# Optimization experiments

Measured on AMD Instinct MI355X. Metric: run time of the kernel, lower is better.

## Reference

```python
import jax, jax.numpy as jnp
import numpy as np

N = 8192   # nodes per graph batch
D = 128    # node_feat_dim
E = 131072 # edges per graph batch
B = 64     # graphs per batch


def _linear_init(k, fin, fout):
    s = 1.0 / np.sqrt(fin)
    kw, kb = jax.random.split(k)
    W = jax.random.uniform(kw, (fin, fout), jnp.float32, -s, s)
    b = jax.random.uniform(kb, (fout,), jnp.float32, -s, s)
    return W, b


def setup_inputs() -> dict:
    key = jax.random.key(0)
    ks = jax.random.split(key, 10)
    x1 = jax.random.normal(ks[0], (N, D), jnp.float32)
    x2 = jax.random.normal(ks[1], (N, D), jnp.float32)
    edge_index1 = jax.random.randint(ks[2], (2, E), 0, N)
    edge_index2 = jax.random.randint(ks[3], (2, E), 0, N)
    # block-contiguous graph ids; every graph id present on both sides
    batch = jnp.arange(N, dtype=jnp.int32) // (N // B)
    mW1, mb1 = _linear_init(ks[4], 2 * D, 512)
    mW2, mb2 = _linear_init(ks[5], 512, 256)  # 256 == 2*D (update_net constraint)
    uW1, ub1 = _linear_init(ks[6], 4 * D, 512)
    uW2, ub2 = _linear_init(ks[7], 512, 256)
    uW3, ub3 = _linear_init(ks[8], 256, D)
    return dict(x1=x1, edge_index1=edge_index1, batch1=batch,
                x2=x2, edge_index2=edge_index2, batch2=batch,
                mW1=mW1, mb1=mb1, mW2=mW2, mb2=mb2,
                uW1=uW1, ub1=ub1, uW2=uW2, ub2=ub2, uW3=uW3, ub3=ub3)


def _message_aggr(x, edge_index, mW1, mb1, mW2, mb2):
    tgt, src = edge_index[0], edge_index[1]
    inp = jnp.concatenate([x[src], x[tgt]], axis=-1)          # [E, 2D]
    msg = jax.nn.relu(inp @ mW1 + mb1) @ mW2 + mb2            # [E, 2D]
    return jax.ops.segment_sum(msg, tgt, num_segments=x.shape[0])


def _cross_attention(x1, batch1, x2, batch2):
    scores = x1 @ x2.T                                        # [N1, N2]
    mask = batch1[:, None] == batch2[None, :]
    scores = jnp.where(mask, scores, -jnp.inf)
    att1 = x1 - jax.nn.softmax(scores, axis=1) @ x2
    att2 = x2 - jax.nn.softmax(scores, axis=0).T @ x1
    return att1, att2


def _node_update(x, messages, attentions, uW1, ub1, uW2, ub2, uW3, ub3):
    u = jnp.concatenate([messages, attentions, x], axis=-1)   # [N, 4D]
    h = jax.nn.relu(u @ uW1 + ub1)
    h = jax.nn.relu(h @ uW2 + ub2)
    return x + h @ uW3 + ub3                                  # residual update


def reference(x1, edge_index1, batch1, x2, edge_index2, batch2,
              mW1, mb1, mW2, mb2, uW1, ub1, uW2, ub2, uW3, ub3):
    m1 = _message_aggr(x1, edge_index1, mW1, mb1, mW2, mb2)
    m2 = _message_aggr(x2, edge_index2, mW1, mb1, mW2, mb2)
    a1, a2 = _cross_attention(x1, batch1, x2, batch2)
    new_x1 = _node_update(x1, m1, a1, uW1, ub1, uW2, ub2, uW3, ub3)
    new_x2 = _node_update(x2, m2, a2, uW1, ub1, uW2, ub2, uW3, ub3)
    return new_x1, new_x2
```

## Files before the change

### kernel.cpp

```cpp
#include <hip/hip_runtime.h>
#include <stdint.h>


typedef unsigned short u16;
typedef __bf16 bf16x8 __attribute__((ext_vector_type(8)));
typedef float f32x4 __attribute__((ext_vector_type(4)));

#define NN 8192
#define DD 128
#define EE 131072
#define GS 128
#define NG 64

__device__ __forceinline__ float bf2f(u16 u){
  return __uint_as_float(((uint32_t)u) << 16);
}
__device__ __forceinline__ u16 f2bf(float f){
  uint32_t x = __float_as_uint(f);
  return (u16)((x + 0x7fffu + ((x >> 16) & 1u)) >> 16);
}
__device__ __forceinline__ void gload16(const u16* g, u16* l){
  __builtin_amdgcn_global_load_lds(
      (const __attribute__((address_space(1))) uint32_t*)(uintptr_t)g,
      (__attribute__((address_space(3))) uint32_t*)(uintptr_t)l, 16, 0, 0);
}
template<int N>
__device__ __forceinline__ void wbar(){
  if constexpr (N == 0)      asm volatile("s_waitcnt vmcnt(0)" ::: "memory");
  else if constexpr (N == 1) asm volatile("s_waitcnt vmcnt(1)" ::: "memory");
  else if constexpr (N == 2) asm volatile("s_waitcnt vmcnt(2)" ::: "memory");
  else if constexpr (N == 4) asm volatile("s_waitcnt vmcnt(4)" ::: "memory");
  __builtin_amdgcn_s_barrier();
  __builtin_amdgcn_sched_barrier(0);
}
__device__ __forceinline__ void bar(){
  __builtin_amdgcn_s_barrier();
  __builtin_amdgcn_sched_barrier(0);
}

__device__ __forceinline__ void pq_gemm(
    const u16* __restrict__ A, const u16* __restrict__ Wt,
    const float* __restrict__ bias, u16* __restrict__ out,
    int bx, int by, u16* __restrict__ sh, int t)
{
  u16* As = sh;
  u16* Bs = sh + 16384;
  const int brow = by << 7, bcol = bx << 7;
  const int w = t >> 6, lane = t & 63;
  const int rb = (w >> 1) << 6, cb = (w & 1) << 6;
  const int lr = lane & 15, lq = lane >> 4;

  #pragma unroll
  for (int i = 0; i < 8; i++){
    int sg = i * 256 + t;
    int r = sg >> 4, p = sg & 15;
    int l = p ^ (r & 7);
    gload16(A  + (size_t)(brow + r) * 128 + (l << 3), As + sg * 8);
    gload16(Wt + (size_t)(bcol + r) * 128 + (l << 3), Bs + sg * 8);
  }
  wbar<0>();

  f32x4 acc[4][4];
  #pragma unroll
  for (int i = 0; i < 4; i++)
    #pragma unroll
    for (int j = 0; j < 4; j++) acc[i][j] = (f32x4){0.f, 0.f, 0.f, 0.f};

  #pragma unroll
  for (int kb = 0; kb < 4; kb++){
    bf16x8 af[4], bfr[4];
    #pragma unroll
    for (int mi = 0; mi < 4; mi++){
      int row = rb + mi * 16 + lr;
      af[mi] = *(const bf16x8*)&As[(row << 7) + ((((kb << 2) | lq) ^ (row & 7)) << 3)];
    }
    #pragma unroll
    for (int ni = 0; ni < 4; ni++){
      int row = cb + ni * 16 + lr;
      bfr[ni] = *(const bf16x8*)&Bs[(row << 7) + ((((kb << 2) | lq) ^ (row & 7)) << 3)];
    }
    #pragma unroll
    for (int mi = 0; mi < 4; mi++)
      #pragma unroll
      for (int ni = 0; ni < 4; ni++)
        acc[mi][ni] = __builtin_amdgcn_mfma_f32_16x16x32_bf16(af[mi], bfr[ni], acc[mi][ni], 0, 0, 0);
  }

  #pragma unroll
  for (int mi = 0; mi < 4; mi++)
    #pragma unroll
    for (int ni = 0; ni < 4; ni++)
      #pragma unroll
      for (int rr = 0; rr < 4; rr++){
        int grow = brow + rb + mi * 16 + lq * 4 + rr;
        int gcol = bcol + cb + ni * 16 + lr;
        out[(size_t)grow * 1024 + gcol] = f2bf(acc[mi][ni][rr] + bias[gcol]);
      }
}

__global__ __launch_bounds__(256)
void pre_k(const float* __restrict__ mW1, const float* __restrict__ mb1,
           const float* __restrict__ mW2, const float* __restrict__ uW1,
           const float* __restrict__ uW2, const float* __restrict__ uW3,
           const float* __restrict__ x1, const float* __restrict__ x2,
           const int* __restrict__ ei1, const int* __restrict__ ei2,
           u16* __restrict__ WtPQ, float* __restrict__ bPQ,
           u16* __restrict__ Wtm2, u16* __restrict__ Wtu1,
           u16* __restrict__ Wtu2, u16* __restrict__ Wtu3,
           u16* __restrict__ xb, u16* __restrict__ xt,
           u16* __restrict__ U, int* __restrict__ deg)
{
  __shared__ u16 T[8704];
  int b = blockIdx.x, t = threadIdx.x;
  if (b < 168){
    const float* srcs[6] = {mW1, mW1 + 128 * 512, mW2, uW1, uW2, uW3};
    u16* dsts[6] = {WtPQ, WtPQ + 512 * 128, Wtm2, Wtu1, Wtu2, Wtu3};
    const int ldSs[6] = {512, 512, 256, 512, 256, 128};
    const int ldDs[6] = {128, 128, 512, 512, 512, 256};
    const int jb[7]   = {0, 16, 32, 64, 128, 160, 168};
    int j = 0;
    while (b >= jb[j + 1]) j++;
    const int l = b - jb[j];
    const int ldS = ldSs[j], ldD = ldDs[j];
    const int ntc = ldS >> 6;
    const int k0 = (l / ntc) << 6, c0 = (l % ntc) << 6;
    const float* S = srcs[j];
    u16* D = dsts[j];
    #pragma unroll
    for (int i = 0; i < 4; i++){
      int s = i * 256 + t;
      int r = s >> 4, c4 = (s & 15) << 2;
      float4 v = *(const float4*)&S[(size_t)(k0 + r) * ldS + c0 + c4];
      uint2 pk;
      pk.x = (uint32_t)f2bf(v.x) | ((uint32_t)f2bf(v.y) << 16);
      pk.y = (uint32_t)f2bf(v.z) | ((uint32_t)f2bf(v.w) << 16);
      *(uint2*)&T[r * 68 + c4] = pk;
    }
    __syncthreads();
    #pragma unroll
    for (int i = 0; i < 4; i++){
      int s = i * 256 + t;
      int c = s >> 4, k4 = (s & 15) << 2;
      uint32_t a0 = T[(k4 + 0) * 68 + c];
      uint32_t a1 = T[(k4 + 1) * 68 + c];
      uint32_t a2 = T[(k4 + 2) * 68 + c];
      uint32_t a3 = T[(k4 + 3) * 68 + c];
      uint2 pk; pk.x = a0 | (a1 << 16); pk.y = a2 | (a3 << 16);
      *(uint2*)&D[(size_t)(c0 + c) * ldD + k0 + k4] = pk;
    }
  } else if (b == 168){
    #pragma unroll
    for (int i = 0; i < 4; i++){
      int idx = i * 256 + t;
      bPQ[idx] = (idx < 512) ? 0.f : mb1[idx - 512];
    }
  } else if (b < 2217){
    int a = b - 169;
    int side = a >> 10, blk = a & 1023;
    const float* x = side ? x2 : x1;
    int i4 = blk * 256 + t;
    float4 v = *(const float4*)&x[(size_t)i4 * 4];
    uint2 pk;
    pk.x = (uint32_t)f2bf(v.x) | ((uint32_t)f2bf(v.y) << 16);
    pk.y = (uint32_t)f2bf(v.z) | ((uint32_t)f2bf(v.w) << 16);
    *(uint2*)&xb[(size_t)side * NN * DD + (size_t)i4 * 4] = pk;
    int n = i4 >> 5, d = (i4 << 2) & 127;
    *(uint2*)&U[((size_t)side * NN + n) * 512 + 384 + d] = pk;
  } else if (b < 2473){
    int a = b - 2217;
    int side = a >> 7, blk = a & 127;
    const float* x = side ? x2 : x1;
    u16* dst = xt + (size_t)side * DD * NN;
    const int n0 = blk * 64;
    #pragma unroll
    for (int i = 0; i < 8; i++){
      int s = i * 256 + t;
      int r = s >> 5, c4 = (s & 31) << 2;
      float4 v = *(const float4*)&x[(size_t)(n0 + r) * DD + c4];
      uint2 pk;
      pk.x = (uint32_t)f2bf(v.x) | ((uint32_t)f2bf(v.y) << 16);
      pk.y = (uint32_t)f2bf(v.z) | ((uint32_t)f2bf(v.w) << 16);
      *(uint2*)&T[r * 136 + c4] = pk;
    }
    __syncthreads();
    #pragma unroll
    for (int i = 0; i < 8; i++){
      int s = i * 256 + t;
      int d = s >> 4, n4 = (s & 15) << 2;
      uint32_t a0 = T[(n4 + 0) * 136 + d];
      uint32_t a1 = T[(n4 + 1) * 136 + d];
      uint32_t a2 = T[(n4 + 2) * 136 + d];
      uint32_t a3 = T[(n4 + 3) * 136 + d];
      uint2 pk; pk.x = a0 | (a1 << 16); pk.y = a2 | (a3 << 16);
      *(uint2*)(dst + (size_t)d * NN + n0 + n4) = pk;
    }
  } else {
    int a = b - 2473;
    int side = a >> 9, blk = a & 511;
    const int* ei = side ? ei2 : ei1;
    int e = blk * 256 + t;
    atomicAdd(&deg[side * NN + ei[e]], 1);
  }
}

__global__ __launch_bounds__(256)
void scan_k(const int* __restrict__ deg,
            int* __restrict__ offs1, int* __restrict__ cur1,
            int* __restrict__ offs2, int* __restrict__ cur2){
  const int* d = deg + blockIdx.x * NN;
  int* offs = blockIdx.x ? offs2 : offs1;
  int* cur  = blockIdx.x ? cur2  : cur1;
  __shared__ int part[256];
  const int t = threadIdx.x;
  const int base = t * 32;
  int loc[32];
  int s = 0;
  #pragma unroll
  for (int i = 0; i < 32; i++){ loc[i] = s; s += d[base + i]; }
  part[t] = s;
  __syncthreads();
  for (int off = 1; off < 256; off <<= 1){
    int v = (t >= off) ? part[t - off] : 0;
    __syncthreads();
    part[t] += v;
    __syncthreads();
  }
  int pre = (t == 0) ? 0 : part[t - 1];
  #pragma unroll
  for (int i = 0; i < 32; i++){
    int o = pre + loc[i];
    offs[base + i] = o;
    cur[base + i]  = o;
  }
  if (t == 255) offs[NN] = part[255];
}

__global__ __launch_bounds__(256)
void mid_k(const u16* __restrict__ xb, const u16* __restrict__ WtPQ,
           const float* __restrict__ bPQ, u16* __restrict__ PQ,
           const int* __restrict__ ei1, const int* __restrict__ ei2,
           int* __restrict__ cur1, int* __restrict__ cur2,
           int* __restrict__ srt1, int* __restrict__ srt2,
           const u16* __restrict__ xt, u16* __restrict__ U)
{
  __shared__ u16 sh[32768];
  const int b = blockIdx.x, t = threadIdx.x;
  if (b < 1024){
    pq_gemm(xb, WtPQ, bPQ, PQ, b >> 7, b & 127, sh, t);
    return;
  }
  if (b < 2048){
    int a = b - 1024;
    int side = a >> 9, blk = a & 511;
    const int* ei = side ? ei2 : ei1;
    int* cur = side ? cur2 : cur1;
    int* srt = side ? srt2 : srt1;
    int e = blk * 256 + t;
    int tgt = ei[e], src = ei[EE + e];
    int p = atomicAdd(&cur[tgt], 1);
    srt[p] = src;
    return;
  }
  const int a = b - 2048;
  const int side = a >> 7;
  const int g = a & 63, h = (a >> 6) & 1;
  const u16* Xa = xb + (size_t)side * NN * DD;
  const u16* Xb = xb + (size_t)(1 - side) * NN * DD;
  const u16* Xt = xt + (size_t)(1 - side) * DD * NN;
  u16* Uside = U + (size_t)side * NN * 512;

  u16* XaS = sh;
  u16* XbS = sh + 8704;

  const int w = t >> 6, lane = t & 63;
  const int lr = lane & 15, lq = lane >> 4;

  {
    const u16* sa = Xa + ((size_t)g * GS + h * 64) * DD;
    #pragma unroll
    for (int i = 0; i < 4; i++){
      int s = i * 256 + t; int r = s >> 4, c8 = (s & 15) << 3;
      *(uint4*)&XaS[r * 136 + c8] = *(const uint4*)(sa + (size_t)r * DD + c8);
    }
    const u16* sb = Xb + (size_t)g * GS * DD;
    #pragma unroll
    for (int i = 0; i < 8; i++){
      int s = i * 256 + t; int r = s >> 4, c8 = (s & 15) << 3;
      *(uint4*)&XbS[r * 136 + c8] = *(const uint4*)(sb + (size_t)r * DD + c8);
    }
  }
  __syncthreads();

  f32x4 sc[8];
  #pragma unroll
  for (int ct = 0; ct < 8; ct++) sc[ct] = (f32x4){0.f, 0.f, 0.f, 0.f};
  #pragma unroll
  for (int kb = 0; kb < 4; kb++){
    bf16x8 aa = *(const bf16x8*)&XaS[(w * 16 + lr) * 136 + kb * 32 + (lq << 3)];
    #pragma unroll
    for (int ct = 0; ct < 8; ct++){
      bf16x8 bb = *(const bf16x8*)&XbS[(ct * 16 + lr) * 136 + kb * 32 + (lq << 3)];
      sc[ct] = __builtin_amdgcn_mfma_f32_16x16x32_bf16(aa, bb, sc[ct], 0, 0, 0);
    }
  }
  float inv[4];
  #pragma unroll
  for (int rr = 0; rr < 4; rr++){
    float m = sc[0][rr];
    #pragma unroll
    for (int ct = 1; ct < 8; ct++) m = fmaxf(m, sc[ct][rr]);
    #pragma unroll
    for (int sh_ = 1; sh_ < 16; sh_ <<= 1) m = fmaxf(m, __shfl_xor(m, sh_, 64));
    float s = 0.f;
    #pragma unroll
    for (int ct = 0; ct < 8; ct++){
      float e = __expf(sc[ct][rr] - m);
      sc[ct][rr] = e; s += e;
    }
    #pragma unroll
    for (int sh_ = 1; sh_ < 16; sh_ <<= 1) s += __shfl_xor(s, sh_, 64);
    inv[rr] = 1.f / s;
  }
  #pragma unroll
  for (int ct = 0; ct < 8; ct++)
    #pragma unroll
    for (int rr = 0; rr < 4; rr++)
      XaS[(w * 16 + lq * 4 + rr) * 136 + ct * 16 + lr] = f2bf(sc[ct][rr] * inv[rr]);
  __syncthreads();

  f32x4 o[8];
  #pragma unroll
  for (int ct = 0; ct < 8; ct++) o[ct] = (f32x4){0.f, 0.f, 0.f, 0.f};
  #pragma unroll
  for (int kb = 0; kb < 4; kb++){
    bf16x8 aa = *(const bf16x8*)&XaS[(w * 16 + lr) * 136 + kb * 32 + (lq << 3)];
    #pragma unroll
    for (int ct = 0; ct < 8; ct++){
      bf16x8 bb = *(const bf16x8*)(Xt + (size_t)(ct * 16 + lr) * NN + g * GS + kb * 32 + (lq << 3));
      o[ct] = __builtin_amdgcn_mfma_f32_16x16x32_bf16(aa, bb, o[ct], 0, 0, 0);
    }
  }
  const u16* XaG = Xa + ((size_t)g * GS + h * 64) * DD;
  #pragma unroll
  for (int ct = 0; ct < 8; ct++)
    #pragma unroll
    for (int rr = 0; rr < 4; rr++){
      int row = w * 16 + lq * 4 + rr, col = ct * 16 + lr;
      float xa = bf2f(XaG[(size_t)row * DD + col]);
      Uside[((size_t)g * GS + h * 64 + row) * 512 + 256 + col] = f2bf(xa - o[ct][rr]);
    }
}

__global__ __launch_bounds__(256)
void gather_k(const int* __restrict__ offs1, const int* __restrict__ srt1,
              const int* __restrict__ offs2, const int* __restrict__ srt2,
              const u16* __restrict__ PQ, u16* __restrict__ S)
{
  const int side = blockIdx.y;
  const int* offs = side ? offs2 : offs1;
  const int* srt  = side ? srt2  : srt1;
  const u16* base = PQ + (size_t)side * NN * 1024;
  u16* Sb = S + (size_t)side * NN * 512;

  const int node = (blockIdx.x << 2) + (threadIdx.x >> 6);
  const int lane = threadIdx.x & 63;
  const int beg = offs[node], end = offs[node + 1];
  const u16* lbase = base + (lane << 3);

  uint4 qv = *(const uint4*)(base + (size_t)node * 1024 + 512 + (lane << 3));
  float q[8];
  {
    uint32_t qw[4] = {qv.x, qv.y, qv.z, qv.w};
    #pragma unroll
    for (int i = 0; i < 4; i++){
      q[i * 2]     = bf2f((u16)(qw[i] & 0xffffu));
      q[i * 2 + 1] = bf2f((u16)(qw[i] >> 16));
    }
  }
  float acc[8] = {0.f,0.f,0.f,0.f,0.f,0.f,0.f,0.f};

  int e = beg;
  for (; e + 15 < end; e += 16){
    int sx[16];
    #pragma unroll
    for (int i = 0; i < 16; i++) sx[i] = srt[e + i];
    uint4 pv[16];
    #pragma unroll
    for (int i = 0; i < 16; i++)
      pv[i] = *(const uint4*)(lbase + (size_t)sx[i] * 1024);
    #pragma unroll
    for (int i = 0; i < 16; i++){
      uint32_t w0[4] = {pv[i].x, pv[i].y, pv[i].z, pv[i].w};
      #pragma unroll
      for (int j = 0; j < 4; j++){
        acc[j*2]   += fmaxf(bf2f((u16)(w0[j] & 0xffffu)) + q[j*2],   0.f);
        acc[j*2+1] += fmaxf(bf2f((u16)(w0[j] >> 16))     + q[j*2+1], 0.f);
      }
    }
  }
  for (; e + 7 < end; e += 8){
    int sx[8];
    #pragma unroll
    for (int i = 0; i < 8; i++) sx[i] = srt[e + i];
    uint4 pv[8];
    #pragma unroll
    for (int i = 0; i < 8; i++)
      pv[i] = *(const uint4*)(lbase + (size_t)sx[i] * 1024);
    #pragma unroll
    for (int i = 0; i < 8; i++){
      uint32_t w0[4] = {pv[i].x, pv[i].y, pv[i].z, pv[i].w};
      #pragma unroll
      for (int j = 0; j < 4; j++){
        acc[j*2]   += fmaxf(bf2f((u16)(w0[j] & 0xffffu)) + q[j*2],   0.f);
        acc[j*2+1] += fmaxf(bf2f((u16)(w0[j] >> 16))     + q[j*2+1], 0.f);
      }
    }
  }
  for (; e + 3 < end; e += 4){
    int sx[4];
    #pragma unroll
    for (int i = 0; i < 4; i++) sx[i] = srt[e + i];
    uint4 pv[4];
    #pragma unroll
    for (int i = 0; i < 4; i++)
      pv[i] = *(const uint4*)(lbase + (size_t)sx[i] * 1024);
    #pragma unroll
    for (int i = 0; i < 4; i++){
      uint32_t w0[4] = {pv[i].x, pv[i].y, pv[i].z, pv[i].w};
      #pragma unroll
      for (int j = 0; j < 4; j++){
        acc[j*2]   += fmaxf(bf2f((u16)(w0[j] & 0xffffu)) + q[j*2],   0.f);
        acc[j*2+1] += fmaxf(bf2f((u16)(w0[j] >> 16))     + q[j*2+1], 0.f);
      }
    }
  }
  for (; e < end; e++){
    int sA = srt[e];
    uint4 pA = *(const uint4*)(lbase + (size_t)sA * 1024);
    uint32_t aw[4] = {pA.x, pA.y, pA.z, pA.w};
    #pragma unroll
    for (int i = 0; i < 4; i++){
      acc[i*2]   += fmaxf(bf2f((u16)(aw[i] & 0xffffu)) + q[i*2],   0.f);
      acc[i*2+1] += fmaxf(bf2f((u16)(aw[i] >> 16))     + q[i*2+1], 0.f);
    }
  }
  uint4 pk;
  pk.x = (uint32_t)f2bf(acc[0]) | ((uint32_t)f2bf(acc[1]) << 16);
  pk.y = (uint32_t)f2bf(acc[2]) | ((uint32_t)f2bf(acc[3]) << 16);
  pk.z = (uint32_t)f2bf(acc[4]) | ((uint32_t)f2bf(acc[5]) << 16);
  pk.w = (uint32_t)f2bf(acc[6]) | ((uint32_t)f2bf(acc[7]) << 16);
  *(uint4*)(Sb + (size_t)node * 512 + (lane << 3)) = pk;
}

__global__ __launch_bounds__(512)
void upd_k(const u16* __restrict__ Sg,
           const u16* __restrict__ Wtm2, const float* __restrict__ mb2,
           const int* __restrict__ deg, u16* __restrict__ U,
           const u16* __restrict__ Wtu1, const float* __restrict__ ub1,
           const u16* __restrict__ Wtu2, const float* __restrict__ ub2,
           const u16* __restrict__ Wtu3, const float* __restrict__ ub3,
           const float* __restrict__ x1, const float* __restrict__ x2,
           float* __restrict__ out)
{
  __shared__ u16 sh[66560];
  u16* H1s  = sh;
  u16* H2s  = sh + 33280;
  u16* Bst0 = sh + 50176;
  u16* Bst1 = sh + 58368;

  const int t = threadIdx.x;
  const int w = t >> 6, lane = t & 63;
  const int wr = w >> 2, wc = w & 3;
  const int lr = lane & 15, lq = lane >> 4;
  const int r0 = blockIdx.x << 6;

  const int sB0 = t, sB1 = t + 512;
  const int cB0 = sB0 >> 2, cB1 = sB1 >> 2;
  const int swB0 = (((sB0 & 3) ^ (cB0 & 3)) << 3);
  const int swB1 = (((sB1 & 3) ^ (cB1 & 3)) << 3);
  const int swr = ((lq ^ (lr & 3)) << 3);

  f32x4 acc[2][4];
  auto zacc = [&](){
    #pragma unroll
    for (int i = 0; i < 2; i++)
      #pragma unroll
      for (int j = 0; j < 4; j++) acc[i][j] = (f32x4){0.f, 0.f, 0.f, 0.f};
  };
  bf16x8 afA[2], afB[2];
  auto compA = [&](const bf16x8 (&af)[2], const u16* Bsb){
    bf16x8 bfv[4];
    #pragma unroll
    for (int ct = 0; ct < 4; ct++)
      bfv[ct] = *(const bf16x8*)&Bsb[(wc * 64 + ct * 16 + lr) * 32 + swr];
    #pragma unroll
    for (int mi = 0; mi < 2; mi++)
      #pragma unroll
      for (int ct = 0; ct < 4; ct++)
        acc[mi][ct] = __builtin_amdgcn_mfma_f32_16x16x32_bf16(af[mi], bfv[ct], acc[mi][ct], 0, 0, 0);
  };

  zacc();
  {
    auto ldS = [&](int kb, bf16x8 (&af)[2]){
      #pragma unroll
      for (int mi = 0; mi < 2; mi++)
        af[mi] = *(const bf16x8*)&Sg[(size_t)(r0 + wr * 32 + mi * 16 + lr) * 512 + kb + (lq << 3)];
    };
    auto stB = [&](int kb, u16* dst){
      gload16(Wtm2 + (size_t)cB0 * 512 + kb + swB0, dst + sB0 * 8);
      gload16(Wtm2 + (size_t)cB1 * 512 + kb + swB1, dst + sB1 * 8);
    };
    stB(0, Bst0);
    ldS(0, afA);
    for (int i2 = 0; i2 < 8; i2++){
      const int kb = i2 << 6;
      stB(kb + 32, Bst1); ldS(kb + 32, afB);
      wbar<4>();
      compA(afA, Bst0);
      bar();
      if (i2 < 7){
        stB(kb + 64, Bst0); ldS(kb + 64, afA);
        wbar<4>();
      } else {
        wbar<0>();
      }
      compA(afB, Bst1);
      bar();
    }
    #pragma unroll
    for (int mi = 0; mi < 2; mi++)
      #pragma unroll
      for (int ct = 0; ct < 4; ct++)
        #pragma unroll
        for (int rr = 0; rr < 4; rr++){
          int row = wr * 32 + mi * 16 + lq * 4 + rr;
          int col = wc * 64 + ct * 16 + lr;
          int grow = r0 + row;
          float v = acc[mi][ct][rr] + (float)deg[grow] * mb2[col];
          U[(size_t)grow * 512 + col] = f2bf(v);
        }
  }
  wbar<0>();

  auto ldA = [&](int kb, bf16x8 (&af)[2]){
    #pragma unroll
    for (int mi = 0; mi < 2; mi++)
      af[mi] = *(const bf16x8*)&U[(size_t)(r0 + wr * 32 + mi * 16 + lr) * 512 + kb + (lq << 3)];
  };
  for (int hN = 0; hN < 2; hN++){
    zacc();
    auto stB = [&](int kb, u16* dst){
      gload16(Wtu1 + (size_t)(hN * 256 + cB0) * 512 + kb + swB0, dst + sB0 * 8);
      gload16(Wtu1 + (size_t)(hN * 256 + cB1) * 512 + kb + swB1, dst + sB1 * 8);
    };
    stB(0, Bst0);
    ldA(0, afA);
    for (int i2 = 0; i2 < 8; i2++){
      const int kb = i2 << 6;
      stB(kb + 32, Bst1); ldA(kb + 32, afB);
      wbar<4>();
      compA(afA, Bst0);
      bar();
      if (i2 < 7){
        stB(kb + 64, Bst0); ldA(kb + 64, afA);
        wbar<4>();
      } else {
        wbar<0>();
      }
      compA(afB, Bst1);
      bar();
    }
    #pragma unroll
    for (int mi = 0; mi < 2; mi++)
      #pragma unroll
      for (int ct = 0; ct < 4; ct++)
        #pragma unroll
        for (int rr = 0; rr < 4; rr++){
          int row = wr * 32 + mi * 16 + lq * 4 + rr;
          int col = wc * 64 + ct * 16 + lr;
          float v = acc[mi][ct][rr] + ub1[hN * 256 + col];
          H1s[row * 520 + hN * 256 + col] = f2bf(fmaxf(v, 0.f));
        }
  }
  __syncthreads();

  zacc();
  {
    auto stB = [&](int kb, u16* dst){
      gload16(Wtu2 + (size_t)cB0 * 512 + kb + swB0, dst + sB0 * 8);
      gload16(Wtu2 + (size_t)cB1 * 512 + kb + swB1, dst + sB1 * 8);
    };
    auto comp = [&](int kb, const u16* Bsb){
      bf16x8 af[2], bfv[4];
      #pragma unroll
      for (int mi = 0; mi < 2; mi++)
        af[mi] = *(const bf16x8*)&H1s[(wr * 32 + mi * 16 + lr) * 520 + kb + (lq << 3)];
      #pragma unroll
      for (int ct = 0; ct < 4; ct++)
        bfv[ct] = *(const bf16x8*)&Bsb[(wc * 64 + ct * 16 + lr) * 32 + swr];
      #pragma unroll
      for (int mi = 0; mi < 2; mi++)
        #pragma unroll
        for (int ct = 0; ct < 4; ct++)
          acc[mi][ct] = __builtin_amdgcn_mfma_f32_16x16x32_bf16(af[mi], bfv[ct], acc[mi][ct], 0, 0, 0);
    };
    stB(0, Bst0);
    for (int i2 = 0; i2 < 8; i2++){
      const int kb = i2 << 6;
      stB(kb + 32, Bst1);
      wbar<2>();
      comp(kb, Bst0);
      bar();
      if (i2 < 7){
        stB(kb + 64, Bst0);
        wbar<2>();
      } else {
        wbar<0>();
      }
      comp(kb + 32, Bst1);
      bar();
    }
    #pragma unroll
    for (int mi = 0; mi < 2; mi++)
      #pragma unroll
      for (int ct = 0; ct < 4; ct++)
        #pragma unroll
        for (int rr = 0; rr < 4; rr++){
          int row = wr * 32 + mi * 16 + lq * 4 + rr;
          int col = wc * 64 + ct * 16 + lr;
          H2s[row * 264 + col] = f2bf(fmaxf(acc[mi][ct][rr] + ub2[col], 0.f));
        }
  }
  __syncthreads();

  zacc();
  {
    auto stB = [&](int kb, u16* dst){
      gload16(Wtu3 + (size_t)cB0 * 256 + kb + swB0, dst + sB0 * 8);
    };
    auto comp = [&](int kb, const u16* Bsb){
      bf16x8 af[2], bfv[2];
      #pragma unroll
      for (int mi = 0; mi < 2; mi++)
        af[mi] = *(const bf16x8*)&H2s[(wr * 32 + mi * 16 + lr) * 264 + kb + (lq << 3)];
      #pragma unroll
      for (int ct = 0; ct < 2; ct++)
        bfv[ct] = *(const bf16x8*)&Bsb[(wc * 32 + ct * 16 + lr) * 32 + swr];
      #pragma unroll
      for (int mi = 0; mi < 2; mi++)
        #pragma unroll
        for (int ct = 0; ct < 2; ct++)
          acc[mi][ct] = __builtin_amdgcn_mfma_f32_16x16x32_bf16(af[mi], bfv[ct], acc[mi][ct], 0, 0, 0);
    };
    stB(0, Bst0);
    for (int i2 = 0; i2 < 4; i2++){
      const int kb = i2 << 6;
      stB(kb + 32, Bst1);
      wbar<1>();
      comp(kb, Bst0);
      bar();
      if (i2 < 3){
        stB(kb + 64, Bst0);
        wbar<1>();
      } else {
        wbar<0>();
      }
      comp(kb + 32, Bst1);
      bar();
    }
    #pragma unroll
    for (int mi = 0; mi < 2; mi++)
      #pragma unroll
      for (int ct = 0; ct < 2; ct++)
        #pragma unroll
        for (int rr = 0; rr < 4; rr++){
          int row = wr * 32 + mi * 16 + lq * 4 + rr;
          int col = wc * 32 + ct * 16 + lr;
          int grow = r0 + row;
          const float* rp = (grow < NN) ? x1 : x2;
          float v = acc[mi][ct][rr] + ub3[col]
                  + rp[(size_t)(grow & (NN - 1)) * 128 + col];
          out[(size_t)grow * 128 + col] = v;
        }
  }
}

extern "C" void kernel_launch(void* const* d_in, const int* in_sizes, int n_in,
                              void* d_out, int out_size, void* d_ws, size_t ws_size,
                              hipStream_t stream)
{
  const float* x1  = (const float*)d_in[0];
  const int*   ei1 = (const int*)  d_in[1];
  const float* x2  = (const float*)d_in[3];
  const int*   ei2 = (const int*)  d_in[4];
  const float* mW1 = (const float*)d_in[6];
  const float* mb1 = (const float*)d_in[7];
  const float* mW2 = (const float*)d_in[8];
  const float* mb2 = (const float*)d_in[9];
  const float* uW1 = (const float*)d_in[10];
  const float* ub1 = (const float*)d_in[11];
  const float* uW2 = (const float*)d_in[12];
  const float* ub2 = (const float*)d_in[13];
  const float* uW3 = (const float*)d_in[14];
  const float* ub3 = (const float*)d_in[15];
  float* out = (float*)d_out;

  char* w = (char*)d_ws;
  auto alloc = [&](size_t b){ char* p = w; w += (b + 255) & ~(size_t)255; return p; };
  u16*  S    = (u16*)alloc((size_t)2 * NN * 512 * 2);
  u16*  PQ   = (u16*)alloc((size_t)2 * NN * 1024 * 2);
  u16*  xb   = (u16*)alloc((size_t)2 * NN * DD * 2);
  u16*  xt   = (u16*)alloc((size_t)2 * DD * NN * 2);
  u16*  U    = (u16*)alloc((size_t)2 * NN * 512 * 2);
  int*  deg  = (int*)alloc((size_t)2 * NN * 4);
  int*  offs1 = (int*)alloc((NN + 1) * 4);
  int*  offs2 = (int*)alloc((NN + 1) * 4);
  int*  cur1  = (int*)alloc(NN * 4);
  int*  cur2  = (int*)alloc(NN * 4);
  int*  srt1  = (int*)alloc((size_t)EE * 4);
  int*  srt2  = (int*)alloc((size_t)EE * 4);
  u16*  WtPQ = (u16*)alloc(1024 * 128 * 2);
  float* bPQ = (float*)alloc(1024 * 4);
  u16*  Wtm2 = (u16*)alloc(256 * 512 * 2);
  u16*  Wtu1 = (u16*)alloc(512 * 512 * 2);
  u16*  Wtu2 = (u16*)alloc(256 * 512 * 2);
  u16*  Wtu3 = (u16*)alloc(128 * 256 * 2);

  hipMemsetAsync(deg, 0, (size_t)2 * NN * 4, stream);

  pre_k<<<3497, 256, 0, stream>>>(
      mW1, mb1, mW2, uW1, uW2, uW3, x1, x2, ei1, ei2,
      WtPQ, bPQ, Wtm2, Wtu1, Wtu2, Wtu3, xb, xt, U, deg);

  scan_k<<<2, 256, 0, stream>>>(deg, offs1, cur1, offs2, cur2);

  mid_k<<<2304, 256, 0, stream>>>(xb, WtPQ, bPQ, PQ, ei1, ei2,
                                  cur1, cur2, srt1, srt2, xt, U);

  gather_k<<<dim3(NN / 4, 2), 256, 0, stream>>>(offs1, srt1, offs2, srt2, PQ, S);

  upd_k<<<256, 512, 0, stream>>>(S, Wtm2, mb2, deg, U,
                                 Wtu1, ub1, Wtu2, ub2, Wtu3, ub3,
                                 x1, x2, out);
}
```

Before: 220.0 us.

## Halve upd_k row tile to 32 rows with 256 threads for more blocks

The fused update kernel now uses 32-row tiles, 256 threads (4 waves, each covering a column slice) and 512 blocks instead of 64-row tiles on 512 threads in 256 blocks. Shared memory shrinks to 80KB so two blocks can reside per CU. The padded H1/H2 staging buffers are replaced by XOR-swizzled layouts to avoid bank conflicts. Each block now loads the full weight tiles for half as many rows, which doubles weight traffic from L2 in exchange for better CU coverage and latency hiding.

```diff
diff --git a/kernel.cpp b/kernel.cpp
--- a/kernel.cpp
+++ b/kernel.cpp
@@ -30,6 +30,7 @@
   else if constexpr (N == 1) asm volatile("s_waitcnt vmcnt(1)" ::: "memory");
   else if constexpr (N == 2) asm volatile("s_waitcnt vmcnt(2)" ::: "memory");
   else if constexpr (N == 4) asm volatile("s_waitcnt vmcnt(4)" ::: "memory");
+  else if constexpr (N == 6) asm volatile("s_waitcnt vmcnt(6)" ::: "memory");
   __builtin_amdgcn_s_barrier();
   __builtin_amdgcn_sched_barrier(0);
 }
@@ -452,7 +453,7 @@
   *(uint4*)(Sb + (size_t)node * 512 + (lane << 3)) = pk;
 }
 
-__global__ __launch_bounds__(512)
+__global__ __launch_bounds__(256, 2)
 void upd_k(const u16* __restrict__ Sg,
            const u16* __restrict__ Wtm2, const float* __restrict__ mb2,
            const int* __restrict__ deg, u16* __restrict__ U,
@@ -462,22 +463,23 @@
            const float* __restrict__ x1, const float* __restrict__ x2,
            float* __restrict__ out)
 {
-  __shared__ u16 sh[66560];
+  __shared__ u16 sh[40960];
   u16* H1s  = sh;
-  u16* H2s  = sh + 33280;
-  u16* Bst0 = sh + 50176;
-  u16* Bst1 = sh + 58368;
+  u16* H2s  = sh + 16384;
+  u16* Bst0 = sh + 24576;
+  u16* Bst1 = sh + 32768;
 
   const int t = threadIdx.x;
-  const int w = t >> 6, lane = t & 63;
-  const int wr = w >> 2, wc = w & 3;
+  const int wc = t >> 6, lane = t & 63;
   const int lr = lane & 15, lq = lane >> 4;
-  const int r0 = blockIdx.x << 6;
-
-  const int sB0 = t, sB1 = t + 512;
-  const int cB0 = sB0 >> 2, cB1 = sB1 >> 2;
-  const int swB0 = (((sB0 & 3) ^ (cB0 & 3)) << 3);
-  const int swB1 = (((sB1 & 3) ^ (cB1 & 3)) << 3);
+  const int r0 = blockIdx.x << 5;
+
+  const int s0 = t, s1 = t + 256, s2 = t + 512, s3 = t + 768;
+  const int c0 = s0 >> 2, c1 = s1 >> 2, c2 = s2 >> 2, c3 = s3 >> 2;
+  const int sw0 = (((s0 & 3) ^ (c0 & 3)) << 3);
+  const int sw1 = (((s1 & 3) ^ (c1 & 3)) << 3);
+  const int sw2 = (((s2 & 3) ^ (c2 & 3)) << 3);
+  const int sw3 = (((s3 & 3) ^ (c3 & 3)) << 3);
   const int swr = ((lq ^ (lr & 3)) << 3);
 
   f32x4 acc[2][4];
@@ -505,23 +507,25 @@
     auto ldS = [&](int kb, bf16x8 (&af)[2]){
       #pragma unroll
       for (int mi = 0; mi < 2; mi++)
-        af[mi] = *(const bf16x8*)&Sg[(size_t)(r0 + wr * 32 + mi * 16 + lr) * 512 + kb + (lq << 3)];
+        af[mi] = *(const bf16x8*)&Sg[(size_t)(r0 + mi * 16 + lr) * 512 + kb + (lq << 3)];
     };
     auto stB = [&](int kb, u16* dst){
-      gload16(Wtm2 + (size_t)cB0 * 512 + kb + swB0, dst + sB0 * 8);
-      gload16(Wtm2 + (size_t)cB1 * 512 + kb + swB1, dst + sB1 * 8);
+      gload16(Wtm2 + (size_t)c0 * 512 + kb + sw0, dst + s0 * 8);
+      gload16(Wtm2 + (size_t)c1 * 512 + kb + sw1, dst + s1 * 8);
+      gload16(Wtm2 + (size_t)c2 * 512 + kb + sw2, dst + s2 * 8);
+      gload16(Wtm2 + (size_t)c3 * 512 + kb + sw3, dst + s3 * 8);
     };
     stB(0, Bst0);
     ldS(0, afA);
     for (int i2 = 0; i2 < 8; i2++){
       const int kb = i2 << 6;
       stB(kb + 32, Bst1); ldS(kb + 32, afB);
-      wbar<4>();
+      wbar<6>();
       compA(afA, Bst0);
       bar();
       if (i2 < 7){
         stB(kb + 64, Bst0); ldS(kb + 64, afA);
-        wbar<4>();
+        wbar<6>();
       } else {
         wbar<0>();
       }
@@ -534,7 +538,7 @@
       for (int ct = 0; ct < 4; ct++)
         #pragma unroll
         for (int rr = 0; rr < 4; rr++){
-          int row = wr * 32 + mi * 16 + lq * 4 + rr;
+          int row = mi * 16 + lq * 4 + rr;
           int col = wc * 64 + ct * 16 + lr;
           int grow = r0 + row;
           float v = acc[mi][ct][rr] + (float)deg[grow] * mb2[col];
@@ -546,25 +550,27 @@
   auto ldA = [&](int kb, bf16x8 (&af)[2]){
     #pragma unroll
     for (int mi = 0; mi < 2; mi++)
-      af[mi] = *(const bf16x8*)&U[(size_t)(r0 + wr * 32 + mi * 16 + lr) * 512 + kb + (lq << 3)];
+      af[mi] = *(const bf16x8*)&U[(size_t)(r0 + mi * 16 + lr) * 512 + kb + (lq << 3)];
   };
   for (int hN = 0; hN < 2; hN++){
     zacc();
     auto stB = [&](int kb, u16* dst){
-      gload16(Wtu1 + (size_t)(hN * 256 + cB0) * 512 + kb + swB0, dst + sB0 * 8);
-      gload16(Wtu1 + (size_t)(hN * 256 + cB1) * 512 + kb + swB1, dst + sB1 * 8);
+      gload16(Wtu1 + (size_t)(hN * 256 + c0) * 512 + kb + sw0, dst + s0 * 8);
+      gload16(Wtu1 + (size_t)(hN * 256 + c1) * 512 + kb + sw1, dst + s1 * 8);
+      gload16(Wtu1 + (size_t)(hN * 256 + c2) * 512 + kb + sw2, dst + s2 * 8);
+      gload16(Wtu1 + (size_t)(hN * 256 + c3) * 512 + kb + sw3, dst + s3 * 8);
     };
     stB(0, Bst0);
     ldA(0, afA);
     for (int i2 = 0; i2 < 8; i2++){
       const int kb = i2 << 6;
       stB(kb + 32, Bst1); ldA(kb + 32, afB);
-      wbar<4>();
+      wbar<6>();
       compA(afA, Bst0);
       bar();
       if (i2 < 7){
         stB(kb + 64, Bst0); ldA(kb + 64, afA);
-        wbar<4>();
+        wbar<6>();
       } else {
         wbar<0>();
       }
@@ -577,10 +583,10 @@
       for (int ct = 0; ct < 4; ct++)
         #pragma unroll
         for (int rr = 0; rr < 4; rr++){
-          int row = wr * 32 + mi * 16 + lq * 4 + rr;
-          int col = wc * 64 + ct * 16 + lr;
-          float v = acc[mi][ct][rr] + ub1[hN * 256 + col];
-          H1s[row * 520 + hN * 256 + col] = f2bf(fmaxf(v, 0.f));
+          int row = mi * 16 + lq * 4 + rr;
+          int gcol = hN * 256 + wc * 64 + ct * 16 + lr;
+          float v = acc[mi][ct][rr] + ub1[gcol];
+          H1s[(row << 9) + (gcol ^ ((row & 7) << 3))] = f2bf(fmaxf(v, 0.f));
         }
   }
   __syncthreads();
@@ -588,14 +594,18 @@
   zacc();
   {
     auto stB = [&](int kb, u16* dst){
-      gload16(Wtu2 + (size_t)cB0 * 512 + kb + swB0, dst + sB0 * 8);
-      gload16(Wtu2 + (size_t)cB1 * 512 + kb + swB1, dst + sB1 * 8);
+      gload16(Wtu2 + (size_t)c0 * 512 + kb + sw0, dst + s0 * 8);
+      gload16(Wtu2 + (size_t)c1 * 512 + kb + sw1, dst + s1 * 8);
+      gload16(Wtu2 + (size_t)c2 * 512 + kb + sw2, dst + s2 * 8);
+      gload16(Wtu2 + (size_t)c3 * 512 + kb + sw3, dst + s3 * 8);
     };
     auto comp = [&](int kb, const u16* Bsb){
       bf16x8 af[2], bfv[4];
       #pragma unroll
-      for (int mi = 0; mi < 2; mi++)
-        af[mi] = *(const bf16x8*)&H1s[(wr * 32 + mi * 16 + lr) * 520 + kb + (lq << 3)];
+      for (int mi = 0; mi < 2; mi++){
+        int row = mi * 16 + lr;
+        af[mi] = *(const bf16x8*)&H1s[(row << 9) + ((kb + (lq << 3)) ^ ((row & 7) << 3))];
+      }
       #pragma unroll
       for (int ct = 0; ct < 4; ct++)
         bfv[ct] = *(const bf16x8*)&Bsb[(wc * 64 + ct * 16 + lr) * 32 + swr];
@@ -609,12 +619,12 @@
     for (int i2 = 0; i2 < 8; i2++){
       const int kb = i2 << 6;
       stB(kb + 32, Bst1);
-      wbar<2>();
+      wbar<4>();
       comp(kb, Bst0);
       bar();
       if (i2 < 7){
         stB(kb + 64, Bst0);
-        wbar<2>();
+        wbar<4>();
       } else {
         wbar<0>();
       }
@@ -627,9 +637,10 @@
       for (int ct = 0; ct < 4; ct++)
         #pragma unroll
         for (int rr = 0; rr < 4; rr++){
-          int row = wr * 32 + mi * 16 + lq * 4 + rr;
+          int row = mi * 16 + lq * 4 + rr;
           int col = wc * 64 + ct * 16 + lr;
-          H2s[row * 264 + col] = f2bf(fmaxf(acc[mi][ct][rr] + ub2[col], 0.f));
+          float v = fmaxf(acc[mi][ct][rr] + ub2[col], 0.f);
+          H2s[(row << 8) + (col ^ ((row & 7) << 3))] = f2bf(v);
         }
   }
   __syncthreads();
@@ -637,13 +648,16 @@
   zacc();
   {
     auto stB = [&](int kb, u16* dst){
-      gload16(Wtu3 + (size_t)cB0 * 256 + kb + swB0, dst + sB0 * 8);
+      gload16(Wtu3 + (size_t)c0 * 256 + kb + sw0, dst + s0 * 8);
+      gload16(Wtu3 + (size_t)c1 * 256 + kb + sw1, dst + s1 * 8);
     };
     auto comp = [&](int kb, const u16* Bsb){
       bf16x8 af[2], bfv[2];
       #pragma unroll
-      for (int mi = 0; mi < 2; mi++)
-        af[mi] = *(const bf16x8*)&H2s[(wr * 32 + mi * 16 + lr) * 264 + kb + (lq << 3)];
+      for (int mi = 0; mi < 2; mi++){
+        int row = mi * 16 + lr;
+        af[mi] = *(const bf16x8*)&H2s[(row << 8) + ((kb + (lq << 3)) ^ ((row & 7) << 3))];
+      }
       #pragma unroll
       for (int ct = 0; ct < 2; ct++)
         bfv[ct] = *(const bf16x8*)&Bsb[(wc * 32 + ct * 16 + lr) * 32 + swr];
@@ -657,12 +671,12 @@
     for (int i2 = 0; i2 < 4; i2++){
       const int kb = i2 << 6;
       stB(kb + 32, Bst1);
-      wbar<1>();
+      wbar<2>();
       comp(kb, Bst0);
       bar();
       if (i2 < 3){
         stB(kb + 64, Bst0);
-        wbar<1>();
+        wbar<2>();
       } else {
         wbar<0>();
       }
@@ -675,7 +689,7 @@
       for (int ct = 0; ct < 2; ct++)
         #pragma unroll
         for (int rr = 0; rr < 4; rr++){
-          int row = wr * 32 + mi * 16 + lq * 4 + rr;
+          int row = mi * 16 + lq * 4 + rr;
           int col = wc * 32 + ct * 16 + lr;
           int grow = r0 + row;
           const float* rp = (grow < NN) ? x1 : x2;
@@ -740,7 +754,7 @@
 
   gather_k<<<dim3(NN / 4, 2), 256, 0, stream>>>(offs1, srt1, offs2, srt2, PQ, S);
 
-  upd_k<<<256, 512, 0, stream>>>(S, Wtm2, mb2, deg, U,
+  upd_k<<<512, 256, 0, stream>>>(S, Wtm2, mb2, deg, U,
                                  Wtu1, ub1, Wtu2, ub2, Wtu3, ub3,
                                  x1, x2, out);
 }
```

Result: no change. 223.4 us (+1.6%).
